# Kernel optimization log

Measured on AMD Instinct MI355X. Metric: run time of the kernel, lower is better.

The kernel has to match this reference:

```python
import jax, jax.numpy as jnp
import numpy as np

D = 128      # dims[0]: number of nodes
M1 = 256     # dims[1]
M2 = 128     # dims[2]
M3 = 1       # dims[3] (must be 1 for final squeeze)
B = 4096     # batch


def setup_inputs() -> dict:
    key = jax.random.key(0)
    ks = jax.random.split(key, 7)
    x = jax.random.normal(ks[0], (B, D), dtype=jnp.float32)
    # nn.Linear(D, D*M1): weight [D*M1, D], bias [D*M1]
    bnd1 = 1.0 / np.sqrt(D)
    W1 = jax.random.uniform(ks[1], (D * M1, D), minval=-bnd1, maxval=bnd1, dtype=jnp.float32)
    b1 = jax.random.uniform(ks[2], (D * M1,), minval=-bnd1, maxval=bnd1, dtype=jnp.float32)
    # An(D, M1, M2): weight [D, M1, M2], bias [D, M2]
    bnd_a = 1.0 / np.sqrt(M1)
    Wa = jax.random.uniform(ks[3], (D, M1, M2), minval=-bnd_a, maxval=bnd_a, dtype=jnp.float32)
    ba = jax.random.uniform(ks[4], (D, M2), minval=-bnd_a, maxval=bnd_a, dtype=jnp.float32)
    # An(D, M2, M3): weight [D, M2, M3], bias [D, M3]
    bnd_b = 1.0 / np.sqrt(M2)
    Wb = jax.random.uniform(ks[5], (D, M2, M3), minval=-bnd_b, maxval=bnd_b, dtype=jnp.float32)
    bb = jax.random.uniform(ks[6], (D, M3), minval=-bnd_b, maxval=bnd_b, dtype=jnp.float32)
    return {"x": x, "W1": W1, "b1": b1, "Wa": Wa, "ba": ba, "Wb": Wb, "bb": bb}


def reference(x, W1, b1, Wa, ba, Wb, bb):
    # a1: [B, D] -> [B, D*M1] -> [B, D, M1]
    h = (x @ W1.T + b1).reshape(B, D, M1)
    # An layer 1: sigmoid then per-node matmul + bias
    h = jnp.einsum('bni,nio->bno', jax.nn.sigmoid(h), Wa) + ba  # [B, D, M2]
    # An layer 2
    h = jnp.einsum('bni,nio->bno', jax.nn.sigmoid(h), Wb) + bb  # [B, D, 1]
    return h.squeeze(axis=2)  # [B, D]
```

## Files before the change

kernel.cpp:

```cpp
#include <hip/hip_runtime.h>
#include <hip/hip_bf16.h>

#define D_NODES 128
#define KD      128
#define M1_     256
#define M2_     128
#define B_      4096
#define BM      256
#define WROWS   64
#define CI      64
#define NCH     4
#define LOG2E   1.44269504088896f

typedef short bf16x8  __attribute__((ext_vector_type(8)));
typedef short short4v __attribute__((ext_vector_type(4)));
typedef float f32x4   __attribute__((ext_vector_type(4)));
typedef unsigned int uint2v __attribute__((ext_vector_type(2)));

#define MFMA16(a, b, c) __builtin_amdgcn_mfma_f32_16x16x32_bf16((a), (b), (c), 0, 0, 0)

__device__ __forceinline__ short f2b(float f) {
  unsigned u = __builtin_bit_cast(unsigned, f);
  u += 0x7FFFu + ((u >> 16) & 1u);
  return (short)(u >> 16);
}

__device__ __forceinline__ float sigmoid_pre(float acc, float bs) {
  float tt = __builtin_fmaf(acc, -LOG2E, bs);
  float e = __builtin_amdgcn_exp2f(tt);
  return __builtin_amdgcn_rcpf(1.0f + e);
}

__device__ __forceinline__ short4v pack_sig4(f32x4 a, f32x4 bs) {
  float s0 = sigmoid_pre(a[0], bs[0]);
  float s1 = sigmoid_pre(a[1], bs[1]);
  float s2 = sigmoid_pre(a[2], bs[2]);
  float s3 = sigmoid_pre(a[3], bs[3]);
  __hip_bfloat162 h01 = __float22bfloat162_rn(make_float2(s0, s1));
  __hip_bfloat162 h23 = __float22bfloat162_rn(make_float2(s2, s3));
  uint2v uv;
  unsigned u0, u1;
  __builtin_memcpy(&u0, &h01, 4);
  __builtin_memcpy(&u1, &h23, 4);
  uv[0] = u0;
  uv[1] = u1;
  return __builtin_bit_cast(short4v, uv);
}

__global__ void cvt_f2b_k(const float* __restrict__ in, short* __restrict__ out) {
  int i = (blockIdx.x * 256 + threadIdx.x) * 4;
  float4 f = *(const float4*)(in + i);
  short4v s; s[0] = f2b(f.x); s[1] = f2b(f.y); s[2] = f2b(f.z); s[3] = f2b(f.w);
  *(short4v*)(out + i) = s;
}

__global__ void trans_wa_k(const float* __restrict__ Wa, short* __restrict__ waT) {
  __shared__ float lt[64][129];
  int node = blockIdx.x >> 2, iblk = blockIdx.x & 3;
  int t = threadIdx.x;
  for (int j = 0; j < 32; ++j) {
    int e = j * 256 + t;
    int i = e >> 7, o = e & 127;
    lt[i][o] = Wa[(node * M1_ + iblk * 64 + i) * M2_ + o];
  }
  __syncthreads();
  int il = t & 63, ob = t >> 6;
  for (int j = 0; j < 32; ++j) {
    int o = j * 4 + ob;
    waT[(node * M2_ + o) * M1_ + iblk * 64 + il] = f2b(lt[il][o]);
  }
}

template <bool FAST>
__global__ __launch_bounds__(256, 1)
void fused_dag_k(const float* __restrict__ x,  const float* __restrict__ W1,
                 const float* __restrict__ b1, const float* __restrict__ Wa,
                 const float* __restrict__ ba, const float* __restrict__ Wb,
                 const float* __restrict__ bb, float* __restrict__ out,
                 const short* __restrict__ w1b, const short* __restrict__ waT,
                 const short* __restrict__ xb) {
  __shared__ __align__(16) short w1s[M1_ * KD];
  __shared__ __align__(16) short was[M2_ * M1_];
  __shared__ __align__(16) short h1w[4 * 16 * CI];

  int gid = blockIdx.x;
  int xcd = gid & 7, ii = gid >> 3;
  int node = xcd * 16 + (ii >> 4);
  int tile = ii & 15;
  int b0 = tile * BM;

  int t = threadIdx.x;
  int w = t >> 6, l = t & 63;
  int n15 = l & 15, q = l >> 4;

  if (FAST) {
    const short* w1n = w1b + (size_t)node * (M1_ * KD);
    const short* wan = waT + (size_t)node * (M2_ * M1_);
    bf16x8 t1[16], t2[16];
#pragma unroll
    for (int j = 0; j < 16; ++j) t1[j] = *(const bf16x8*)(w1n + (j * 256 + t) * 8);
#pragma unroll
    for (int j = 0; j < 16; ++j) t2[j] = *(const bf16x8*)(wan + (j * 256 + t) * 8);
#pragma unroll
    for (int j = 0; j < 16; ++j) {
      int s = j * 256 + t;
      int row = s >> 4, g = s & 15;
      *(bf16x8*)(&w1s[row * KD + ((g ^ (row & 7)) << 3)]) = t1[j];
    }
#pragma unroll
    for (int j = 0; j < 16; ++j) {
      int s = j * 256 + t;
      int row = s >> 5, g = s & 31;
      *(bf16x8*)(&was[row * M1_ + ((g ^ (row & 7)) << 3)]) = t2[j];
    }
  } else {
#pragma unroll
    for (int j = 0; j < 16; ++j) {
      int s = j * 256 + t;
      int row = s >> 4, g = s & 15;
      const float* src = W1 + ((size_t)node * M1_ + row) * KD + g * 8;
      float4 f0 = *(const float4*)(src);
      float4 f1 = *(const float4*)(src + 4);
      bf16x8 v;
      v[0] = f2b(f0.x); v[1] = f2b(f0.y); v[2] = f2b(f0.z); v[3] = f2b(f0.w);
      v[4] = f2b(f1.x); v[5] = f2b(f1.y); v[6] = f2b(f1.z); v[7] = f2b(f1.w);
      *(bf16x8*)(&w1s[row * KD + ((g ^ (row & 7)) << 3)]) = v;
    }
    for (int j = 0; j < 16; ++j) {
      int s = j * 256 + t;
      int o = s >> 5, g = s & 31;
      bf16x8 v;
#pragma unroll
      for (int e = 0; e < 8; ++e)
        v[e] = f2b(Wa[((size_t)node * M1_ + g * 8 + e) * M2_ + o]);
      *(bf16x8*)(&was[o * M1_ + ((g ^ (o & 7)) << 3)]) = v;
    }
  }

  bf16x8 xa[4][4];
  {
    int rb = b0 + w * WROWS;
#pragma unroll
    for (int mt = 0; mt < 4; ++mt) {
      int row = rb + mt * 16 + n15;
#pragma unroll
      for (int kk = 0; kk < 4; ++kk) {
        int k0 = kk * 32 + q * 8;
        if (FAST) {
          xa[mt][kk] = *(const bf16x8*)(xb + row * KD + k0);
        } else {
          float4 f0 = *(const float4*)(x + row * KD + k0);
          float4 f1 = *(const float4*)(x + row * KD + k0 + 4);
          bf16x8 v;
          v[0] = f2b(f0.x); v[1] = f2b(f0.y); v[2] = f2b(f0.z); v[3] = f2b(f0.w);
          v[4] = f2b(f1.x); v[5] = f2b(f1.y); v[6] = f2b(f1.z); v[7] = f2b(f1.w);
          xa[mt][kk] = v;
        }
      }
    }
  }

  __syncthreads();

  int swz = n15 & 7;
  int hsw = (swz >> 2) << 6;
  int qx16 = (q ^ (swz & 3)) << 4;
  int swd32 = (swz >> 1) << 5;
  int qhx = ((q >> 1) ^ (swz & 1)) << 4;
  int qlo8 = (q & 1) << 3;

  const char* w1c8 = (const char*)w1s;
  const char* wac8 = (const char*)was;
  char* h1c8 = (char*)h1w;

  int w1o = n15 * 256 + qx16 + hsw;
  int wao = n15 * 512 + qx16 + hsw;
  int h1wo = w * 2048 + n15 * 128 + qlo8 + qhx + swd32;
  int h1ro = w * 2048 + n15 * 128 + qx16 + hsw;

  f32x4 acc2[4][8];
#pragma unroll
  for (int a = 0; a < 4; ++a)
#pragma unroll
    for (int b = 0; b < 8; ++b) acc2[a][b] = (f32x4){0.f, 0.f, 0.f, 0.f};

  const float* b1n = b1 + node * M1_;

  for (int c = 0; c < NCH; ++c) {
    bf16x8 wf[4][4];
    int w1base = w1o + c * 16384;
#pragma unroll
    for (int kk = 0; kk < 4; ++kk) {
      int p = w1base ^ (kk << 6);
#pragma unroll
      for (int it = 0; it < 4; ++it)
        wf[it][kk] = *(const bf16x8*)(w1c8 + p + it * 4096);
    }
    bf16x8 wa[8][2];
    int wabase = wao + c * 128;
#pragma unroll
    for (int kk = 0; kk < 2; ++kk) {
      int p = wabase ^ (kk << 6);
#pragma unroll
      for (int ot = 0; ot < 8; ++ot)
        wa[ot][kk] = *(const bf16x8*)(wac8 + p + ot * 8192);
    }

    const float* b1c = b1n + c * CI;
    f32x4 bs[4];
#pragma unroll
    for (int it = 0; it < 4; ++it)
      bs[it] = (*(const f32x4*)(b1c + it * 16 + q * 4)) * (-LOG2E);

    f32x4 acc1[4];
#pragma unroll
    for (int a = 0; a < 4; ++a) acc1[a] = (f32x4){0.f, 0.f, 0.f, 0.f};
#pragma unroll
    for (int kk = 0; kk < 4; ++kk)
#pragma unroll
      for (int it = 0; it < 4; ++it)
        acc1[it] = MFMA16(wf[it][kk], xa[0][kk], acc1[it]);

#pragma unroll
    for (int mt = 0; mt < 4; ++mt) {
      short4v s4[4];
#pragma unroll
      for (int it = 0; it < 4; ++it) s4[it] = pack_sig4(acc1[it], bs[it]);
#pragma unroll
      for (int it = 0; it < 4; ++it)
        *(short4v*)(h1c8 + (h1wo ^ (it << 5))) = s4[it];
      bf16x8 ha[2];
#pragma unroll
      for (int kk = 0; kk < 2; ++kk)
        ha[kk] = *(const bf16x8*)(h1c8 + (h1ro ^ (kk << 6)));

      if (mt < 3) {
#pragma unroll
        for (int a = 0; a < 4; ++a) acc1[a] = (f32x4){0.f, 0.f, 0.f, 0.f};
#pragma unroll
        for (int kk = 0; kk < 4; ++kk)
#pragma unroll
          for (int it = 0; it < 4; ++it)
            acc1[it] = MFMA16(wf[it][kk], xa[mt + 1][kk], acc1[it]);
      }

#pragma unroll
      for (int kk = 0; kk < 2; ++kk)
#pragma unroll
        for (int ot = 0; ot < 8; ++ot)
          acc2[mt][ot] = MFMA16(ha[kk], wa[ot][kk], acc2[mt][ot]);
    }
  }

  const float* ban = ba + node * M2_;
  const float* wbn = Wb + node * M2_;
  float bbv = bb[node];
  float bas[8], wbs[8];
#pragma unroll
  for (int ot = 0; ot < 8; ++ot) {
    int o = ot * 16 + n15;
    bas[ot] = ban[o] * (-LOG2E);
    wbs[ot] = wbn[o];
  }
#pragma unroll
  for (int mt = 0; mt < 4; ++mt) {
    f32x4 rs = (f32x4){0.f, 0.f, 0.f, 0.f};
#pragma unroll
    for (int ot = 0; ot < 8; ++ot)
#pragma unroll
      for (int r = 0; r < 4; ++r)
        rs[r] += sigmoid_pre(acc2[mt][ot][r], bas[ot]) * wbs[ot];
#pragma unroll
    for (int r = 0; r < 4; ++r) {
      float v = rs[r];
      v += __shfl_xor(v, 1);
      v += __shfl_xor(v, 2);
      v += __shfl_xor(v, 4);
      v += __shfl_xor(v, 8);
      if (n15 == 0)
        out[(size_t)(b0 + w * WROWS + mt * 16 + q * 4 + r) * D_NODES + node] = v + bbv;
    }
  }
}

extern "C" void kernel_launch(void* const* d_in, const int* in_sizes, int n_in,
                              void* d_out, int out_size, void* d_ws, size_t ws_size,
                              hipStream_t stream) {
  const float* x  = (const float*)d_in[0];
  const float* W1 = (const float*)d_in[1];
  const float* b1 = (const float*)d_in[2];
  const float* Wa = (const float*)d_in[3];
  const float* ba = (const float*)d_in[4];
  const float* Wb = (const float*)d_in[5];
  const float* bb = (const float*)d_in[6];
  float* out = (float*)d_out;

  const size_t W1_ELEMS = (size_t)D_NODES * M1_ * KD;
  const size_t WA_ELEMS = (size_t)D_NODES * M1_ * M2_;
  const size_t X_ELEMS  = (size_t)B_ * KD;
  const size_t NEED = (W1_ELEMS + WA_ELEMS + X_ELEMS) * sizeof(short);

  const int GRID = D_NODES * (B_ / BM);

  if (ws_size >= NEED) {
    short* w1b = (short*)d_ws;
    short* waT = w1b + W1_ELEMS;
    short* xb  = waT + WA_ELEMS;
    cvt_f2b_k<<<(int)(W1_ELEMS / 1024), 256, 0, stream>>>(W1, w1b);
    cvt_f2b_k<<<(int)(X_ELEMS / 1024), 256, 0, stream>>>(x, xb);
    trans_wa_k<<<D_NODES * 4, 256, 0, stream>>>(Wa, waT);
    fused_dag_k<true><<<GRID, 256, 0, stream>>>(x, W1, b1, Wa, ba, Wb, bb, out,
                                                w1b, waT, xb);
  } else {
    fused_dag_k<false><<<GRID, 256, 0, stream>>>(x, W1, b1, Wa, ba, Wb, bb, out,
                                                 nullptr, nullptr, nullptr);
  }
}
```

Before: 155.5 us.

## Shrink per-block LDS and registers to run several 512-thread blocks per CU

```diff
diff --git a/kernel.cpp b/kernel.cpp
--- a/kernel.cpp
+++ b/kernel.cpp
@@ -6,8 +6,7 @@
 #define M1_     256
 #define M2_     128
 #define B_      4096
-#define BM      256
-#define WROWS   64
+#define BM      128
 #define CI      64
 #define NCH     4
 #define LOG2E   1.44269504088896f
@@ -72,95 +71,44 @@
 }
 
 template <bool FAST>
-__global__ __launch_bounds__(256, 1)
+__global__ __launch_bounds__(512, 4)
 void fused_dag_k(const float* __restrict__ x,  const float* __restrict__ W1,
                  const float* __restrict__ b1, const float* __restrict__ Wa,
                  const float* __restrict__ ba, const float* __restrict__ Wb,
                  const float* __restrict__ bb, float* __restrict__ out,
                  const short* __restrict__ w1b, const short* __restrict__ waT,
                  const short* __restrict__ xb) {
-  __shared__ __align__(16) short w1s[M1_ * KD];
-  __shared__ __align__(16) short was[M2_ * M1_];
-  __shared__ __align__(16) short h1w[4 * 16 * CI];
+  __shared__ __align__(16) short w1s[128 * KD];
+  __shared__ __align__(16) short h1w[8 * 16 * CI];
 
   int gid = blockIdx.x;
   int xcd = gid & 7, ii = gid >> 3;
-  int node = xcd * 16 + (ii >> 4);
-  int tile = ii & 15;
+  int node = xcd * 16 + (ii >> 5);
+  int tile = ii & 31;
   int b0 = tile * BM;
 
   int t = threadIdx.x;
   int w = t >> 6, l = t & 63;
   int n15 = l & 15, q = l >> 4;
 
-  if (FAST) {
-    const short* w1n = w1b + (size_t)node * (M1_ * KD);
-    const short* wan = waT + (size_t)node * (M2_ * M1_);
-    bf16x8 t1[16], t2[16];
-#pragma unroll
-    for (int j = 0; j < 16; ++j) t1[j] = *(const bf16x8*)(w1n + (j * 256 + t) * 8);
-#pragma unroll
-    for (int j = 0; j < 16; ++j) t2[j] = *(const bf16x8*)(wan + (j * 256 + t) * 8);
-#pragma unroll
-    for (int j = 0; j < 16; ++j) {
-      int s = j * 256 + t;
-      int row = s >> 4, g = s & 15;
-      *(bf16x8*)(&w1s[row * KD + ((g ^ (row & 7)) << 3)]) = t1[j];
+  bf16x8 xa[4];
+  {
+    int row = b0 + w * 16 + n15;
+#pragma unroll
+    for (int kk = 0; kk < 4; ++kk) {
+      int k0 = kk * 32 + q * 8;
+      if (FAST) {
+        xa[kk] = *(const bf16x8*)(xb + row * KD + k0);
+      } else {
+        float4 f0 = *(const float4*)(x + row * KD + k0);
+        float4 f1 = *(const float4*)(x + row * KD + k0 + 4);
+        bf16x8 v;
+        v[0] = f2b(f0.x); v[1] = f2b(f0.y); v[2] = f2b(f0.z); v[3] = f2b(f0.w);
+        v[4] = f2b(f1.x); v[5] = f2b(f1.y); v[6] = f2b(f1.z); v[7] = f2b(f1.w);
+        xa[kk] = v;
+      }
     }
-#pragma unroll
-    for (int j = 0; j < 16; ++j) {
-      int s = j * 256 + t;
-      int row = s >> 5, g = s & 31;
-      *(bf16x8*)(&was[row * M1_ + ((g ^ (row & 7)) << 3)]) = t2[j];
-    }
-  } else {
-#pragma unroll
-    for (int j = 0; j < 16; ++j) {
-      int s = j * 256 + t;
-      int row = s >> 4, g = s & 15;
-      const float* src = W1 + ((size_t)node * M1_ + row) * KD + g * 8;
-      float4 f0 = *(const float4*)(src);
-      float4 f1 = *(const float4*)(src + 4);
-      bf16x8 v;
-      v[0] = f2b(f0.x); v[1] = f2b(f0.y); v[2] = f2b(f0.z); v[3] = f2b(f0.w);
-      v[4] = f2b(f1.x); v[5] = f2b(f1.y); v[6] = f2b(f1.z); v[7] = f2b(f1.w);
-      *(bf16x8*)(&w1s[row * KD + ((g ^ (row & 7)) << 3)]) = v;
-    }
-    for (int j = 0; j < 16; ++j) {
-      int s = j * 256 + t;
-      int o = s >> 5, g = s & 31;
-      bf16x8 v;
-#pragma unroll
-      for (int e = 0; e < 8; ++e)
-        v[e] = f2b(Wa[((size_t)node * M1_ + g * 8 + e) * M2_ + o]);
-      *(bf16x8*)(&was[o * M1_ + ((g ^ (o & 7)) << 3)]) = v;
-    }
-  }
-
-  bf16x8 xa[4][4];
-  {
-    int rb = b0 + w * WROWS;
-#pragma unroll
-    for (int mt = 0; mt < 4; ++mt) {
-      int row = rb + mt * 16 + n15;
-#pragma unroll
-      for (int kk = 0; kk < 4; ++kk) {
-        int k0 = kk * 32 + q * 8;
-        if (FAST) {
-          xa[mt][kk] = *(const bf16x8*)(xb + row * KD + k0);
-        } else {
-          float4 f0 = *(const float4*)(x + row * KD + k0);
-          float4 f1 = *(const float4*)(x + row * KD + k0 + 4);
-          bf16x8 v;
-          v[0] = f2b(f0.x); v[1] = f2b(f0.y); v[2] = f2b(f0.z); v[3] = f2b(f0.w);
-          v[4] = f2b(f1.x); v[5] = f2b(f1.y); v[6] = f2b(f1.z); v[7] = f2b(f1.w);
-          xa[mt][kk] = v;
-        }
-      }
-    }
-  }
-
-  __syncthreads();
+  }
 
   int swz = n15 & 7;
   int hsw = (swz >> 2) << 6;
@@ -170,62 +118,104 @@
   int qlo8 = (q & 1) << 3;
 
   const char* w1c8 = (const char*)w1s;
-  const char* wac8 = (const char*)was;
   char* h1c8 = (char*)h1w;
 
   int w1o = n15 * 256 + qx16 + hsw;
-  int wao = n15 * 512 + qx16 + hsw;
   int h1wo = w * 2048 + n15 * 128 + qlo8 + qhx + swd32;
   int h1ro = w * 2048 + n15 * 128 + qx16 + hsw;
 
-  f32x4 acc2[4][8];
-#pragma unroll
-  for (int a = 0; a < 4; ++a)
-#pragma unroll
-    for (int b = 0; b < 8; ++b) acc2[a][b] = (f32x4){0.f, 0.f, 0.f, 0.f};
-
+  const short* w1n = w1b + (size_t)node * (M1_ * KD);
+  const short* wan = waT + (size_t)node * (M2_ * M1_);
   const float* b1n = b1 + node * M1_;
 
-  for (int c = 0; c < NCH; ++c) {
-    bf16x8 wf[4][4];
-    int w1base = w1o + c * 16384;
-#pragma unroll
-    for (int kk = 0; kk < 4; ++kk) {
-      int p = w1base ^ (kk << 6);
+  f32x4 acc2[8];
+#pragma unroll
+  for (int b = 0; b < 8; ++b) acc2[b] = (f32x4){0.f, 0.f, 0.f, 0.f};
+
+  for (int h = 0; h < 2; ++h) {
+    if (h) __syncthreads();
+    if (FAST) {
+#pragma unroll
+      for (int j = 0; j < 4; ++j) {
+        int s = j * 512 + t;
+        int row = s >> 4, g = s & 15;
+        bf16x8 v = *(const bf16x8*)(w1n + (h * 128 + row) * KD + g * 8);
+        *(bf16x8*)(&w1s[row * KD + ((g ^ (row & 7)) << 3)]) = v;
+      }
+    } else {
+#pragma unroll
+      for (int j = 0; j < 4; ++j) {
+        int s = j * 512 + t;
+        int row = s >> 4, g = s & 15;
+        const float* src = W1 + ((size_t)node * M1_ + h * 128 + row) * KD + g * 8;
+        float4 f0 = *(const float4*)(src);
+        float4 f1 = *(const float4*)(src + 4);
+        bf16x8 v;
+        v[0] = f2b(f0.x); v[1] = f2b(f0.y); v[2] = f2b(f0.z); v[3] = f2b(f0.w);
+        v[4] = f2b(f1.x); v[5] = f2b(f1.y); v[6] = f2b(f1.z); v[7] = f2b(f1.w);
+        *(bf16x8*)(&w1s[row * KD + ((g ^ (row & 7)) << 3)]) = v;
+      }
+    }
+    __syncthreads();
+
+    for (int cl = 0; cl < 2; ++cl) {
+      int c = h * 2 + cl;
+
+      bf16x8 wa0[8];
+#pragma unroll
+      for (int ot = 0; ot < 8; ++ot) {
+        if (FAST) {
+          wa0[ot] = *(const bf16x8*)(wan + (ot * 16 + n15) * M1_ + c * CI + q * 8);
+        } else {
+          bf16x8 v;
+#pragma unroll
+          for (int e = 0; e < 8; ++e)
+            v[e] = f2b(Wa[((size_t)node * M1_ + c * CI + q * 8 + e) * M2_ +
+                          (ot * 16 + n15)]);
+          wa0[ot] = v;
+        }
+      }
+
+      f32x4 bs[4];
+      const float* b1c = b1n + c * CI;
 #pragma unroll
       for (int it = 0; it < 4; ++it)
-        wf[it][kk] = *(const bf16x8*)(w1c8 + p + it * 4096);
-    }
-    bf16x8 wa[8][2];
-    int wabase = wao + c * 128;
-#pragma unroll
-    for (int kk = 0; kk < 2; ++kk) {
-      int p = wabase ^ (kk << 6);
-#pragma unroll
-      for (int ot = 0; ot < 8; ++ot)
-        wa[ot][kk] = *(const bf16x8*)(wac8 + p + ot * 8192);
-    }
-
-    const float* b1c = b1n + c * CI;
-    f32x4 bs[4];
-#pragma unroll
-    for (int it = 0; it < 4; ++it)
-      bs[it] = (*(const f32x4*)(b1c + it * 16 + q * 4)) * (-LOG2E);
-
-    f32x4 acc1[4];
-#pragma unroll
-    for (int a = 0; a < 4; ++a) acc1[a] = (f32x4){0.f, 0.f, 0.f, 0.f};
-#pragma unroll
-    for (int kk = 0; kk < 4; ++kk)
-#pragma unroll
-      for (int it = 0; it < 4; ++it)
-        acc1[it] = MFMA16(wf[it][kk], xa[0][kk], acc1[it]);
-
-#pragma unroll
-    for (int mt = 0; mt < 4; ++mt) {
+        bs[it] = (*(const f32x4*)(b1c + it * 16 + q * 4)) * (-LOG2E);
+
+      f32x4 acc1[4];
+#pragma unroll
+      for (int a = 0; a < 4; ++a) acc1[a] = (f32x4){0.f, 0.f, 0.f, 0.f};
+      int w1base = w1o + cl * 16384;
+#pragma unroll
+      for (int kk = 0; kk < 4; ++kk) {
+        int p = w1base ^ (kk << 6);
+#pragma unroll
+        for (int it = 0; it < 4; ++it) {
+          bf16x8 wf = *(const bf16x8*)(w1c8 + p + it * 4096);
+          acc1[it] = MFMA16(wf, xa[kk], acc1[it]);
+        }
+      }
+
       short4v s4[4];
 #pragma unroll
       for (int it = 0; it < 4; ++it) s4[it] = pack_sig4(acc1[it], bs[it]);
+
+      bf16x8 wa1[8];
+#pragma unroll
+      for (int ot = 0; ot < 8; ++ot) {
+        if (FAST) {
+          wa1[ot] =
+              *(const bf16x8*)(wan + (ot * 16 + n15) * M1_ + c * CI + 32 + q * 8);
+        } else {
+          bf16x8 v;
+#pragma unroll
+          for (int e = 0; e < 8; ++e)
+            v[e] = f2b(Wa[((size_t)node * M1_ + c * CI + 32 + q * 8 + e) * M2_ +
+                          (ot * 16 + n15)]);
+          wa1[ot] = v;
+        }
+      }
+
 #pragma unroll
       for (int it = 0; it < 4; ++it)
         *(short4v*)(h1c8 + (h1wo ^ (it << 5))) = s4[it];
@@ -234,52 +224,37 @@
       for (int kk = 0; kk < 2; ++kk)
         ha[kk] = *(const bf16x8*)(h1c8 + (h1ro ^ (kk << 6)));
 
-      if (mt < 3) {
-#pragma unroll
-        for (int a = 0; a < 4; ++a) acc1[a] = (f32x4){0.f, 0.f, 0.f, 0.f};
-#pragma unroll
-        for (int kk = 0; kk < 4; ++kk)
-#pragma unroll
-          for (int it = 0; it < 4; ++it)
-            acc1[it] = MFMA16(wf[it][kk], xa[mt + 1][kk], acc1[it]);
-      }
-
-#pragma unroll
-      for (int kk = 0; kk < 2; ++kk)
-#pragma unroll
-        for (int ot = 0; ot < 8; ++ot)
-          acc2[mt][ot] = MFMA16(ha[kk], wa[ot][kk], acc2[mt][ot]);
+#pragma unroll
+      for (int ot = 0; ot < 8; ++ot)
+        acc2[ot] = MFMA16(ha[0], wa0[ot], acc2[ot]);
+#pragma unroll
+      for (int ot = 0; ot < 8; ++ot)
+        acc2[ot] = MFMA16(ha[1], wa1[ot], acc2[ot]);
     }
   }
 
   const float* ban = ba + node * M2_;
   const float* wbn = Wb + node * M2_;
   float bbv = bb[node];
-  float bas[8], wbs[8];
+  f32x4 rs = (f32x4){0.f, 0.f, 0.f, 0.f};
 #pragma unroll
   for (int ot = 0; ot < 8; ++ot) {
     int o = ot * 16 + n15;
-    bas[ot] = ban[o] * (-LOG2E);
-    wbs[ot] = wbn[o];
-  }
-#pragma unroll
-  for (int mt = 0; mt < 4; ++mt) {
-    f32x4 rs = (f32x4){0.f, 0.f, 0.f, 0.f};
-#pragma unroll
-    for (int ot = 0; ot < 8; ++ot)
-#pragma unroll
-      for (int r = 0; r < 4; ++r)
-        rs[r] += sigmoid_pre(acc2[mt][ot][r], bas[ot]) * wbs[ot];
-#pragma unroll
-    for (int r = 0; r < 4; ++r) {
-      float v = rs[r];
-      v += __shfl_xor(v, 1);
-      v += __shfl_xor(v, 2);
-      v += __shfl_xor(v, 4);
-      v += __shfl_xor(v, 8);
-      if (n15 == 0)
-        out[(size_t)(b0 + w * WROWS + mt * 16 + q * 4 + r) * D_NODES + node] = v + bbv;
-    }
+    float bav = ban[o] * (-LOG2E);
+    float wbv = wbn[o];
+#pragma unroll
+    for (int r = 0; r < 4; ++r)
+      rs[r] += sigmoid_pre(acc2[ot][r], bav) * wbv;
+  }
+#pragma unroll
+  for (int r = 0; r < 4; ++r) {
+    float v = rs[r];
+    v += __shfl_xor(v, 1);
+    v += __shfl_xor(v, 2);
+    v += __shfl_xor(v, 4);
+    v += __shfl_xor(v, 8);
+    if (n15 == 0)
+      out[(size_t)(b0 + w * 16 + q * 4 + r) * D_NODES + node] = v + bbv;
   }
 }
 
@@ -309,10 +284,10 @@
     cvt_f2b_k<<<(int)(W1_ELEMS / 1024), 256, 0, stream>>>(W1, w1b);
     cvt_f2b_k<<<(int)(X_ELEMS / 1024), 256, 0, stream>>>(x, xb);
     trans_wa_k<<<D_NODES * 4, 256, 0, stream>>>(Wa, waT);
-    fused_dag_k<true><<<GRID, 256, 0, stream>>>(x, W1, b1, Wa, ba, Wb, bb, out,
+    fused_dag_k<true><<<GRID, 512, 0, stream>>>(x, W1, b1, Wa, ba, Wb, bb, out,
                                                 w1b, waT, xb);
   } else {
-    fused_dag_k<false><<<GRID, 256, 0, stream>>>(x, W1, b1, Wa, ba, Wb, bb, out,
+    fused_dag_k<false><<<GRID, 512, 0, stream>>>(x, W1, b1, Wa, ba, Wb, bb, out,
                                                  nullptr, nullptr, nullptr);
   }
 }
```

Result: slower. 300.8 us (+93.4%).
